# Optimization experiments

Measured on AMD Instinct MI355X. Metric: run time of the kernel, lower is better.

## Reference

```python
import jax, jax.numpy as jnp
import numpy as np

B, T, D = 2, 1024, 1024
H, DH = 16, 64          # d_head = d_model // n_heads
MAX_POS = 64


def setup_inputs() -> dict:
    key = jax.random.key(0)
    ks = jax.random.split(key, 11)
    s = 1.0 / np.sqrt(D)
    x = jax.random.normal(ks[0], (B, T, D), jnp.float32)
    Wq = jax.random.normal(ks[1], (D, D), jnp.float32) * s
    Wk = jax.random.normal(ks[2], (D, D), jnp.float32) * s
    Wv = jax.random.normal(ks[3], (D, D), jnp.float32) * s
    Wo = jax.random.normal(ks[4], (D, D), jnp.float32) * s
    bq = jnp.zeros((D,), jnp.float32)
    bk = jnp.zeros((D,), jnp.float32)
    bv = jnp.zeros((D,), jnp.float32)
    bo = jnp.zeros((D,), jnp.float32)
    pos_emb = jax.random.normal(ks[5], (H, MAX_POS, DH), jnp.float32) * 0.02
    causal_mask = jnp.triu(jnp.ones((T, T), bool), k=1)  # True = masked (j > i)
    return dict(x=x, Wq=Wq, bq=bq, Wk=Wk, bk=bk, Wv=Wv, bv=bv, Wo=Wo, bo=bo,
                pos_emb=pos_emb, causal_mask=causal_mask)


def reference(x, Wq, bq, Wk, bk, Wv, bv, Wo, bo, pos_emb, causal_mask):
    Bv, Tv, _ = x.shape
    scale = np.sqrt(DH).astype(np.float32)

    def proj(W, b):
        return (x @ W.T + b).reshape(Bv, Tv, H, DH).transpose(0, 2, 1, 3)  # (B,H,T,d)

    Q, K, V = proj(Wq, bq), proj(Wk, bk), proj(Wv, bv)

    qk = jnp.einsum('bhid,bhjd->bhij', Q, K)              # (B,H,T,T)
    gates = jax.nn.sigmoid(qk / scale)
    gates = jnp.where(causal_mask, 0.0, gates)
    cum = jnp.cumsum(gates, axis=-1)
    pos = cum[..., -1:] - cum                             # total - cumsum_left

    pos = jnp.clip(pos, 0.0, MAX_POS - 1.0)
    pos_floor = jnp.floor(pos)
    alpha = (pos - pos_floor)[..., None]                  # (B,H,T,T,1) -> broadcast
    fidx = pos_floor.astype(jnp.int32)
    cidx = jnp.clip(jnp.ceil(pos), 0, MAX_POS - 1).astype(jnp.int32)

    # q_i . PE_{i,j} via precomputed q.pos_emb table (same math, no (B,H,T,T,d) tensor)
    qpe_tab = jnp.einsum('bhid,hpd->bhip', Q, pos_emb)    # (B,H,T,MAX_POS)
    qpe_f = jnp.take_along_axis(qpe_tab, fidx, axis=-1)   # (B,H,T,T)
    qpe_c = jnp.take_along_axis(qpe_tab, cidx, axis=-1)
    q_pe = (1.0 - alpha[..., 0]) * qpe_f + alpha[..., 0] * qpe_c

    scores = (qk + q_pe) / scale
    scores = jnp.where(causal_mask, -jnp.inf, scores)
    attn = jax.nn.softmax(scores, axis=-1)

    out = jnp.einsum('bhij,bhjd->bhid', attn, V)
    out = out.transpose(0, 2, 1, 3).reshape(Bv, Tv, D)
    return out @ Wo.T + bo
```

## Files before the change

kernel.cpp:

```cpp
#include <hip/hip_runtime.h>
#include <math.h>

#define Tt 1024
#define Dd 1024
#define Hh 16
#define DHh 64
#define MAXPOS 64
#define BTt 2048

typedef short short8 __attribute__((ext_vector_type(8)));
typedef float floatx4 __attribute__((ext_vector_type(4)));

#define MFMA16 __builtin_amdgcn_mfma_f32_16x16x32_bf16

__device__ __forceinline__ unsigned short f2bf(float f) {
    unsigned u;
    __builtin_memcpy(&u, &f, 4);
    u = (u + 0x7FFFu + ((u >> 16) & 1u)) >> 16;
    return (unsigned short)u;
}
__device__ __forceinline__ float bf2fs(short s) {
    unsigned u = ((unsigned)(unsigned short)s) << 16;
    float f;
    __builtin_memcpy(&f, &u, 4);
    return f;
}
__device__ __forceinline__ float fsigm(float x) {
    return __builtin_amdgcn_rcpf(1.f + __expf(-x));
}

__global__ __launch_bounds__(256) void conv_bf16(
    const float* __restrict__ x,  const float* __restrict__ W0,
    const float* __restrict__ W1, const float* __restrict__ W2,
    const float* __restrict__ W3,
    short* __restrict__ xb, short* __restrict__ w0b, short* __restrict__ w1b,
    short* __restrict__ w2b, short* __restrict__ w3b)
{
    const float* src; short* dst; int n;
    switch (blockIdx.y) {
        case 0:  src = x;  dst = xb;  n = BTt * Dd; break;
        case 1:  src = W0; dst = w0b; n = Dd * Dd;  break;
        case 2:  src = W1; dst = w1b; n = Dd * Dd;  break;
        case 3:  src = W2; dst = w2b; n = Dd * Dd;  break;
        default: src = W3; dst = w3b; n = Dd * Dd;  break;
    }
    int idx = (blockIdx.x * 256 + threadIdx.x) * 8;
    if (idx >= n) return;
    floatx4 a0 = *(const floatx4*)&src[idx];
    floatx4 a1 = *(const floatx4*)&src[idx + 4];
    short8 s;
    for (int e = 0; e < 4; ++e) {
        s[e]     = (short)f2bf(a0[e]);
        s[e + 4] = (short)f2bf(a1[e]);
    }
    *(short8*)&dst[idx] = s;
}

#define BM 128
#define BN 128
#define BKK 64
#define LDSS 72

template <int MODE>
__device__ __forceinline__ void gemm_body(const short* __restrict__ A,
                                          const short* __restrict__ W,
                                          const float* __restrict__ bias,
                                          void* __restrict__ Cout,
                                          int N, int K)
{
    __shared__ __align__(16) short Ash[BM * LDSS];
    __shared__ __align__(16) short Bsh[BN * LDSS];
    const int t = threadIdx.x;
    const int lane = t & 63, wave = t >> 6;
    const int wm = wave >> 1, wn = wave & 1;
    const int quad = lane >> 4, l16 = lane & 15;
    const int row0 = blockIdx.x * BM, col0 = blockIdx.y * BN;

    floatx4 acc[4][4];
    for (int a = 0; a < 4; ++a)
        for (int b2 = 0; b2 < 4; ++b2)
            acc[a][b2] = (floatx4){0.f, 0.f, 0.f, 0.f};

    for (int kb = 0; kb < K; kb += BKK) {
        __syncthreads();
        for (int q2 = 0; q2 < 4; ++q2) {
            int ch = t + 256 * q2;
            int r = ch >> 3, c = ch & 7;
            *(short8*)&Ash[r * LDSS + c * 8] =
                *(const short8*)&A[(size_t)(row0 + r) * K + kb + c * 8];
            *(short8*)&Bsh[r * LDSS + c * 8] =
                *(const short8*)&W[(size_t)(col0 + r) * K + kb + c * 8];
        }
        __syncthreads();
        for (int ks = 0; ks < BKK / 32; ++ks) {
            short8 af[4], bfr[4];
            for (int tm = 0; tm < 4; ++tm)
                af[tm] = *(short8*)&Ash[(wm * 64 + tm * 16 + l16) * LDSS + ks * 32 + quad * 8];
            for (int tn = 0; tn < 4; ++tn)
                bfr[tn] = *(short8*)&Bsh[(wn * 64 + tn * 16 + l16) * LDSS + ks * 32 + quad * 8];
            for (int tm = 0; tm < 4; ++tm)
                for (int tn = 0; tn < 4; ++tn)
                    acc[tm][tn] = MFMA16(af[tm], bfr[tn], acc[tm][tn], 0, 0, 0);
        }
    }
    for (int tm = 0; tm < 4; ++tm)
        for (int tn = 0; tn < 4; ++tn) {
            int col = col0 + wn * 64 + tn * 16 + l16;
            float bv = bias[col];
            for (int r = 0; r < 4; ++r) {
                int row = row0 + wm * 64 + tm * 16 + quad * 4 + r;
                float v = acc[tm][tn][r] + bv;
                if (MODE == 0) ((float*)Cout)[(size_t)row * N + col] = v;
                else           ((short*)Cout)[(size_t)row * N + col] = (short)f2bf(v);
            }
        }
}

__global__ __launch_bounds__(256) void gemm_qkv(
    const short* __restrict__ xb,
    const short* __restrict__ Wqb, const short* __restrict__ Wkb,
    const short* __restrict__ Wvb,
    const float* __restrict__ bq, const float* __restrict__ bk,
    const float* __restrict__ bv,
    short* __restrict__ Qb, short* __restrict__ Kb, short* __restrict__ Vrow)
{
    if (blockIdx.z == 0)      gemm_body<1>(xb, Wqb, bq, Qb, Dd, Dd);
    else if (blockIdx.z == 1) gemm_body<1>(xb, Wkb, bk, Kb, Dd, Dd);
    else                      gemm_body<1>(xb, Wvb, bv, Vrow, Dd, Dd);
}

__global__ __launch_bounds__(256) void gemm_o(
    const short* __restrict__ A, const short* __restrict__ W,
    const float* __restrict__ bias, float* __restrict__ C)
{
    gemm_body<0>(A, W, bias, C, Dd, Dd);
}

__global__ __launch_bounds__(256) void vt_gates(
    const short* __restrict__ Q, const short* __restrict__ K,
    const short* __restrict__ Vrow, short* __restrict__ Vt,
    float* __restrict__ gts)
{
    __shared__ __align__(16) short Qt[32 * 72];
    __shared__ __align__(16) short KV[128 * 72];
    __shared__ float redg[32 * 4];

    const int t = threadIdx.x;

    if (blockIdx.x >= 256) {
        const int j0 = (blockIdx.x - 256) * 64, d0 = blockIdx.y * 64, b = blockIdx.z;
        short* L = KV;
        for (int s = 0; s < 2; ++s) {
            int c = t * 2 + s;
            int jr = c >> 3, c8 = c & 7;
            *(short8*)&L[jr * 72 + c8 * 8] =
                *(const short8*)&Vrow[((size_t)(b * Tt + j0 + jr)) * Dd + d0 + c8 * 8];
        }
        __syncthreads();
        for (int s = 0; s < 2; ++s) {
            int c = t * 2 + s;
            int dr = c >> 3, c8 = c & 7;
            short8 v;
            for (int e = 0; e < 8; ++e) v[e] = L[(c8 * 8 + e) * 72 + dr];
            *(short8*)&Vt[((size_t)(b * Dd + d0 + dr)) * Tt + j0 + c8 * 8] = v;
        }
        return;
    }

    const int it = blockIdx.x >> 3, jt = blockIdx.x & 7;
    const int h = blockIdx.y, b = blockIdx.z;
    const int i0 = it * 32, j0 = jt * 128;
    const int lane = t & 63, wave = t >> 6;
    const int quad = lane >> 4, l16 = lane & 15;

    float* g = &gts[(((size_t)(b * Hh + h)) * Tt + i0) * 8 + jt];
    if (j0 > i0 + 31) {
        if (t < 32) g[t * 8] = 0.f;
        return;
    }

    const float inv_scale = 0.125f;

    {
        int r = t >> 3, c = t & 7;
        *(short8*)&Qt[r * 72 + c * 8] =
            *(const short8*)&Q[((size_t)(b * Tt + i0 + r)) * Dd + h * DHh + c * 8];
    }
    for (int e = 0; e < 4; ++e) {
        int ch = t + 256 * e;
        int jr = ch >> 3, c = ch & 7;
        *(short8*)&KV[jr * 72 + c * 8] =
            *(const short8*)&K[((size_t)(b * Tt + j0 + jr)) * Dd + h * DHh + c * 8];
    }
    __syncthreads();

    int ntA = 2 * wave, ntB = ntA + 1;
    floatx4 c00 = {0,0,0,0}, c01 = {0,0,0,0}, c10 = {0,0,0,0}, c11 = {0,0,0,0};
    for (int ks = 0; ks < 2; ++ks) {
        short8 a0 = *(short8*)&Qt[(l16) * 72 + ks * 32 + quad * 8];
        short8 a1 = *(short8*)&Qt[(16 + l16) * 72 + ks * 32 + quad * 8];
        short8 b0 = *(short8*)&KV[(ntA * 16 + l16) * 72 + ks * 32 + quad * 8];
        short8 b1 = *(short8*)&KV[(ntB * 16 + l16) * 72 + ks * 32 + quad * 8];
        c00 = MFMA16(a0, b0, c00, 0, 0, 0);
        c01 = MFMA16(a0, b1, c01, 0, 0, 0);
        c10 = MFMA16(a1, b0, c10, 0, 0, 0);
        c11 = MFMA16(a1, b1, c11, 0, 0, 0);
    }
    const int jA = j0 + ntA * 16 + l16;
    const int jB = j0 + ntB * 16 + l16;
    for (int r = 0; r < 4; ++r) {
        int m0 = i0 + quad * 4 + r;
        int m1 = m0 + 16;
        float v0 = ((jA <= m0) ? fsigm(c00[r] * inv_scale) : 0.f)
                 + ((jB <= m0) ? fsigm(c01[r] * inv_scale) : 0.f);
        float v1 = ((jA <= m1) ? fsigm(c10[r] * inv_scale) : 0.f)
                 + ((jB <= m1) ? fsigm(c11[r] * inv_scale) : 0.f);
        for (int o = 1; o < 16; o <<= 1) {
            v0 += __shfl_xor(v0, o, 64);
            v1 += __shfl_xor(v1, o, 64);
        }
        if (l16 == 0) {
            redg[(quad * 4 + r) * 4 + wave]      = v0;
            redg[(16 + quad * 4 + r) * 4 + wave] = v1;
        }
    }
    __syncthreads();
    if (t < 32) {
        float s2 = redg[t * 4] + redg[t * 4 + 1] + redg[t * 4 + 2] + redg[t * 4 + 3];
        g[t * 8] = s2;
    }
}

__global__ __launch_bounds__(256) void cope_attn(
    const short* __restrict__ Q, const short* __restrict__ K,
    const short* __restrict__ Vt, const float* __restrict__ PE,
    const float* __restrict__ gts, short* __restrict__ AOb)
{
    const int h = blockIdx.y, b = blockIdx.z;
    const int t = threadIdx.x, lane = t & 63, wave = t >> 6;
    const int quad = lane >> 4, l16 = lane & 15;

    __shared__ __align__(16) short SldS[32 * 264];
    __shared__ __align__(16) short KV[128 * 72];
    __shared__ short qpeB[32 * 68];
    __shared__ float lrow[32];
    float* Sld = (float*)SldS;

    const float inv_scale = 0.125f;
    const int sr = t >> 3, ss = t & 7;

    for (int phase = 0; phase < 2; ++phase) {
        const int it = (phase == 0) ? (31 - (int)blockIdx.x) : (int)blockIdx.x;
        const int i0 = it * 32;
        const int irow = i0 + sr;

        float grow[8];
        {
            const float* gp = &gts[(((size_t)(b * Hh + h)) * Tt + i0 + sr) * 8];
            for (int k = 0; k < 8; ++k) grow[k] = gp[k];
        }
        float tot = 0.f;
        for (int k = 0; k < 8; ++k) tot += grow[k];

        short* QtS = SldS;
        {
            int r = t >> 3, c = t & 7;
            *(short8*)&QtS[r * 72 + c * 8] =
                *(const short8*)&Q[((size_t)(b * Tt + i0 + r)) * Dd + h * DHh + c * 8];
        }
        for (int e = 0; e < 16; ++e) {
            int idx = t + 256 * e;
            int p = idx >> 6, d = idx & 63;
            KV[p * 72 + d] = (short)f2bf(PE[((size_t)h * MAXPOS + p) * DHh + d]);
        }
        __syncthreads();

        short8 qa[2][2];
        for (int rb = 0; rb < 2; ++rb)
            for (int ks = 0; ks < 2; ++ks)
                qa[rb][ks] = *(short8*)&QtS[(rb * 16 + l16) * 72 + ks * 32 + quad * 8];

        {
            int mt = wave >> 1;
            int ntA = 2 * (wave & 1), ntB = ntA + 1;
            floatx4 c0f = {0, 0, 0, 0}, c1f = {0, 0, 0, 0};
            for (int ks = 0; ks < 2; ++ks) {
                short8 b0 = *(short8*)&KV[(ntA * 16 + l16) * 72 + ks * 32 + quad * 8];
                short8 b1 = *(short8*)&KV[(ntB * 16 + l16) * 72 + ks * 32 + quad * 8];
                c0f = MFMA16(qa[mt][ks], b0, c0f, 0, 0, 0);
                c1f = MFMA16(qa[mt][ks], b1, c1f, 0, 0, 0);
            }
            for (int r = 0; r < 4; ++r) {
                qpeB[(mt * 16 + quad * 4 + r) * 68 + ntA * 16 + l16] = (short)f2bf(c0f[r]);
                qpeB[(mt * 16 + quad * 4 + r) * 68 + ntB * 16 + l16] = (short)f2bf(c1f[r]);
            }
        }

        const int JT = (i0 + 159) >> 7;
        floatx4 o0 = {0, 0, 0, 0}, o1 = {0, 0, 0, 0};
        const int pv_mt = wave >> 1;
        const int pv_ntA = 2 * (wave & 1), pv_ntB = pv_ntA + 1;
        float l_acc = 0.f;
        float baseAcc = 0.f;

        short8 kreg[4];
        for (int e = 0; e < 4; ++e) {
            int ch = t + 256 * e;
            int jr = ch >> 3, c = ch & 7;
            kreg[e] = *(const short8*)&K[((size_t)(b * Tt + jr)) * Dd + h * DHh + c * 8];
        }

        for (int jt = 0; jt < JT; ++jt) {
            const int j0 = jt * 128;
            __syncthreads();
            for (int e = 0; e < 4; ++e) {
                int ch = t + 256 * e;
                int jr = ch >> 3, c = ch & 7;
                *(short8*)&KV[jr * 72 + c * 8] = kreg[e];
            }
            __syncthreads();
            {
                int ntA = 2 * wave, ntB = ntA + 1;
                floatx4 c00 = {0,0,0,0}, c01 = {0,0,0,0}, c10 = {0,0,0,0}, c11 = {0,0,0,0};
                for (int ks = 0; ks < 2; ++ks) {
                    short8 b0 = *(short8*)&KV[(ntA * 16 + l16) * 72 + ks * 32 + quad * 8];
                    short8 b1 = *(short8*)&KV[(ntB * 16 + l16) * 72 + ks * 32 + quad * 8];
                    c00 = MFMA16(qa[0][ks], b0, c00, 0, 0, 0);
                    c01 = MFMA16(qa[0][ks], b1, c01, 0, 0, 0);
                    c10 = MFMA16(qa[1][ks], b0, c10, 0, 0, 0);
                    c11 = MFMA16(qa[1][ks], b1, c11, 0, 0, 0);
                }
                for (int r = 0; r < 4; ++r) {
                    Sld[(quad * 4 + r) * 132 + ntA * 16 + l16] = c00[r];
                    Sld[(quad * 4 + r) * 132 + ntB * 16 + l16] = c01[r];
                    Sld[(16 + quad * 4 + r) * 132 + ntA * 16 + l16] = c10[r];
                    Sld[(16 + quad * 4 + r) * 132 + ntB * 16 + l16] = c11[r];
                }
            }
            __syncthreads();
            short8 vreg[4];
            for (int e = 0; e < 4; ++e) {
                int ch = t + 256 * e;
                int d = ch >> 4, c = ch & 15;
                vreg[e] = *(const short8*)&Vt[((size_t)(b * Dd + h * DHh + d)) * Tt + j0 + c * 8];
            }
            if (jt + 1 < JT) {
                for (int e = 0; e < 4; ++e) {
                    int ch = t + 256 * e;
                    int jr = ch >> 3, c = ch & 7;
                    kreg[e] = *(const short8*)&K[((size_t)(b * Tt + j0 + 128 + jr)) * Dd + h * DHh + c * 8];
                }
            }
            {
                floatx4 qv[4];
                for (int q4 = 0; q4 < 4; ++q4) {
                    short8 qraw = *(short8*)&SldS[sr * 264 + ss * 32 + q4 * 8];
                    __builtin_memcpy(&qv[q4], &qraw, 16);
                }
                float gt[16];
                float gs = 0.f;
                for (int e = 0; e < 16; ++e) {
                    int j = j0 + ss * 16 + e;
                    float qk = qv[e >> 2][e & 3];
                    float g = (j <= irow) ? fsigm(qk * inv_scale) : 0.f;
                    gt[e] = g;
                    gs += g;
                }
                float inc = gs;
                for (int d2 = 1; d2 < 8; d2 <<= 1) {
                    float n = __shfl_up(inc, d2, 64);
                    if ((lane & 7) >= d2) inc += n;
                }
                float base = baseAcc + (inc - gs);
                float run = 0.f;
                short8 p0, p1;
                for (int e = 0; e < 16; ++e) {
                    run += gt[e];
                    int j = j0 + ss * 16 + e;
                    float pos = tot - (base + run);
                    pos = fminf(fmaxf(pos, 0.f), 63.f);
                    float pf = floorf(pos);
                    float al = pos - pf;
                    int fi = (int)pf;
                    int ci = fi + 1; if (ci > 63) ci = 63;
                    float qp = (1.f - al) * bf2fs(qpeB[sr * 68 + fi]) + al * bf2fs(qpeB[sr * 68 + ci]);
                    float qk = qv[e >> 2][e & 3];
                    float p = (j <= irow) ? __expf((qk + qp) * inv_scale) : 0.f;
                    if (e < 8) p0[e] = (short)f2bf(p); else p1[e - 8] = (short)f2bf(p);
                    l_acc += p;
                }
                *(short8*)&SldS[sr * 264 + ss * 32]     = p0;
                *(short8*)&SldS[sr * 264 + ss * 32 + 8] = p1;
                baseAcc += grow[jt];
            }
            for (int e = 0; e < 4; ++e) {
                int ch = t + 256 * e;
                int d = ch >> 4, c = ch & 15;
                *(short8*)&KV[d * 136 + c * 8] = vreg[e];
            }
            __syncthreads();
            for (int ks = 0; ks < 4; ++ks) {
                short8 a  = *(short8*)&SldS[(pv_mt * 16 + l16) * 264 + ks * 64
                                            + ((quad >> 1) << 5) + ((quad & 1) << 3)];
                short8 b0 = *(short8*)&KV[(pv_ntA * 16 + l16) * 136 + ks * 32 + quad * 8];
                short8 b1 = *(short8*)&KV[(pv_ntB * 16 + l16) * 136 + ks * 32 + quad * 8];
                o0 = MFMA16(a, b0, o0, 0, 0, 0);
                o1 = MFMA16(a, b1, o1, 0, 0, 0);
            }
        }
        float lr = l_acc;
        for (int d2 = 4; d2 >= 1; d2 >>= 1) lr += __shfl_xor(lr, d2, 64);
        if (ss == 0) lrow[sr] = lr;
        __syncthreads();
        for (int r = 0; r < 4; ++r) {
            int row = pv_mt * 16 + quad * 4 + r;
            float inv = __builtin_amdgcn_rcpf(lrow[row]);
            size_t off = ((size_t)(b * Tt + i0 + row)) * Dd + h * DHh;
            AOb[off + pv_ntA * 16 + l16] = (short)f2bf(o0[r] * inv);
            AOb[off + pv_ntB * 16 + l16] = (short)f2bf(o1[r] * inv);
        }
    }
}

extern "C" void kernel_launch(void* const* d_in, const int* in_sizes, int n_in,
                              void* d_out, int out_size, void* d_ws, size_t ws_size,
                              hipStream_t stream)
{
    const float* x  = (const float*)d_in[0];
    const float* Wq = (const float*)d_in[1];
    const float* bq = (const float*)d_in[2];
    const float* Wk = (const float*)d_in[3];
    const float* bk = (const float*)d_in[4];
    const float* Wv = (const float*)d_in[5];
    const float* bv = (const float*)d_in[6];
    const float* Wo = (const float*)d_in[7];
    const float* bo = (const float*)d_in[8];
    const float* pe = (const float*)d_in[9];

    short* xb   = (short*)d_ws;
    short* Wqb  = xb   + (size_t)BTt * Dd;
    short* Wkb  = Wqb  + (size_t)Dd * Dd;
    short* Wvb  = Wkb  + (size_t)Dd * Dd;
    short* Wob  = Wvb  + (size_t)Dd * Dd;
    short* Qb   = Wob  + (size_t)Dd * Dd;
    short* Kb   = Qb   + (size_t)BTt * Dd;
    short* Vrow = Kb   + (size_t)BTt * Dd;
    short* Vtg  = Vrow + (size_t)BTt * Dd;
    short* AOb  = Vtg  + (size_t)BTt * Dd;
    float* gts  = (float*)(AOb + (size_t)BTt * Dd);

    dim3 gc(BTt * Dd / 8 / 256, 5);
    conv_bf16<<<gc, 256, 0, stream>>>(x, Wq, Wk, Wv, Wo, xb, Wqb, Wkb, Wvb, Wob);

    dim3 gq(BTt / BM, Dd / BN, 3);
    gemm_qkv<<<gq, 256, 0, stream>>>(xb, Wqb, Wkb, Wvb, bq, bk, bv, Qb, Kb, Vrow);

    dim3 gg(272, Hh, 2);
    vt_gates<<<gg, 256, 0, stream>>>(Qb, Kb, Vrow, Vtg, gts);

    dim3 ga(Tt / 32 / 2, Hh, 2);
    cope_attn<<<ga, 256, 0, stream>>>(Qb, Kb, Vtg, pe, gts, AOb);

    dim3 go(BTt / BM, Dd / BN, 1);
    gemm_o<<<go, 256, 0, stream>>>(AOb, Wob, bo, (float*)d_out);
}
```

Baseline: 200.9 us.

## Iterate key tiles right-to-left to compute suffix gate sums inline

```diff
diff --git a/kernel.cpp b/kernel.cpp
--- a/kernel.cpp
+++ b/kernel.cpp
@@ -136,105 +136,32 @@
     gemm_body<0>(A, W, bias, C, Dd, Dd);
 }
 
-__global__ __launch_bounds__(256) void vt_gates(
-    const short* __restrict__ Q, const short* __restrict__ K,
-    const short* __restrict__ Vrow, short* __restrict__ Vt,
-    float* __restrict__ gts)
-{
-    __shared__ __align__(16) short Qt[32 * 72];
-    __shared__ __align__(16) short KV[128 * 72];
-    __shared__ float redg[32 * 4];
-
+__global__ __launch_bounds__(256) void v_transpose(
+    const short* __restrict__ Vrow, short* __restrict__ Vt)
+{
+    __shared__ __align__(16) short L[64 * 72];
     const int t = threadIdx.x;
-
-    if (blockIdx.x >= 256) {
-        const int j0 = (blockIdx.x - 256) * 64, d0 = blockIdx.y * 64, b = blockIdx.z;
-        short* L = KV;
-        for (int s = 0; s < 2; ++s) {
-            int c = t * 2 + s;
-            int jr = c >> 3, c8 = c & 7;
-            *(short8*)&L[jr * 72 + c8 * 8] =
-                *(const short8*)&Vrow[((size_t)(b * Tt + j0 + jr)) * Dd + d0 + c8 * 8];
-        }
-        __syncthreads();
-        for (int s = 0; s < 2; ++s) {
-            int c = t * 2 + s;
-            int dr = c >> 3, c8 = c & 7;
-            short8 v;
-            for (int e = 0; e < 8; ++e) v[e] = L[(c8 * 8 + e) * 72 + dr];
-            *(short8*)&Vt[((size_t)(b * Dd + d0 + dr)) * Tt + j0 + c8 * 8] = v;
-        }
-        return;
-    }
-
-    const int it = blockIdx.x >> 3, jt = blockIdx.x & 7;
-    const int h = blockIdx.y, b = blockIdx.z;
-    const int i0 = it * 32, j0 = jt * 128;
-    const int lane = t & 63, wave = t >> 6;
-    const int quad = lane >> 4, l16 = lane & 15;
-
-    float* g = &gts[(((size_t)(b * Hh + h)) * Tt + i0) * 8 + jt];
-    if (j0 > i0 + 31) {
-        if (t < 32) g[t * 8] = 0.f;
-        return;
-    }
-
-    const float inv_scale = 0.125f;
-
-    {
-        int r = t >> 3, c = t & 7;
-        *(short8*)&Qt[r * 72 + c * 8] =
-            *(const short8*)&Q[((size_t)(b * Tt + i0 + r)) * Dd + h * DHh + c * 8];
-    }
-    for (int e = 0; e < 4; ++e) {
-        int ch = t + 256 * e;
-        int jr = ch >> 3, c = ch & 7;
-        *(short8*)&KV[jr * 72 + c * 8] =
-            *(const short8*)&K[((size_t)(b * Tt + j0 + jr)) * Dd + h * DHh + c * 8];
+    const int j0 = blockIdx.x * 64, d0 = blockIdx.y * 64, b = blockIdx.z;
+    for (int s = 0; s < 2; ++s) {
+        int c = t * 2 + s;
+        int jr = c >> 3, c8 = c & 7;
+        *(short8*)&L[jr * 72 + c8 * 8] =
+            *(const short8*)&Vrow[((size_t)(b * Tt + j0 + jr)) * Dd + d0 + c8 * 8];
     }
     __syncthreads();
-
-    int ntA = 2 * wave, ntB = ntA + 1;
-    floatx4 c00 = {0,0,0,0}, c01 = {0,0,0,0}, c10 = {0,0,0,0}, c11 = {0,0,0,0};
-    for (int ks = 0; ks < 2; ++ks) {
-        short8 a0 = *(short8*)&Qt[(l16) * 72 + ks * 32 + quad * 8];
-        short8 a1 = *(short8*)&Qt[(16 + l16) * 72 + ks * 32 + quad * 8];
-        short8 b0 = *(short8*)&KV[(ntA * 16 + l16) * 72 + ks * 32 + quad * 8];
-        short8 b1 = *(short8*)&KV[(ntB * 16 + l16) * 72 + ks * 32 + quad * 8];
-        c00 = MFMA16(a0, b0, c00, 0, 0, 0);
-        c01 = MFMA16(a0, b1, c01, 0, 0, 0);
-        c10 = MFMA16(a1, b0, c10, 0, 0, 0);
-        c11 = MFMA16(a1, b1, c11, 0, 0, 0);
-    }
-    const int jA = j0 + ntA * 16 + l16;
-    const int jB = j0 + ntB * 16 + l16;
-    for (int r = 0; r < 4; ++r) {
-        int m0 = i0 + quad * 4 + r;
-        int m1 = m0 + 16;
-        float v0 = ((jA <= m0) ? fsigm(c00[r] * inv_scale) : 0.f)
-                 + ((jB <= m0) ? fsigm(c01[r] * inv_scale) : 0.f);
-        float v1 = ((jA <= m1) ? fsigm(c10[r] * inv_scale) : 0.f)
-                 + ((jB <= m1) ? fsigm(c11[r] * inv_scale) : 0.f);
-        for (int o = 1; o < 16; o <<= 1) {
-            v0 += __shfl_xor(v0, o, 64);
-            v1 += __shfl_xor(v1, o, 64);
-        }
-        if (l16 == 0) {
-            redg[(quad * 4 + r) * 4 + wave]      = v0;
-            redg[(16 + quad * 4 + r) * 4 + wave] = v1;
-        }
-    }
-    __syncthreads();
-    if (t < 32) {
-        float s2 = redg[t * 4] + redg[t * 4 + 1] + redg[t * 4 + 2] + redg[t * 4 + 3];
-        g[t * 8] = s2;
+    for (int s = 0; s < 2; ++s) {
+        int c = t * 2 + s;
+        int dr = c >> 3, c8 = c & 7;
+        short8 v;
+        for (int e = 0; e < 8; ++e) v[e] = L[(c8 * 8 + e) * 72 + dr];
+        *(short8*)&Vt[((size_t)(b * Dd + d0 + dr)) * Tt + j0 + c8 * 8] = v;
     }
 }
 
 __global__ __launch_bounds__(256) void cope_attn(
     const short* __restrict__ Q, const short* __restrict__ K,
     const short* __restrict__ Vt, const float* __restrict__ PE,
-    const float* __restrict__ gts, short* __restrict__ AOb)
+    short* __restrict__ AOb)
 {
     const int h = blockIdx.y, b = blockIdx.z;
     const int t = threadIdx.x, lane = t & 63, wave = t >> 6;
@@ -253,14 +180,6 @@
         const int it = (phase == 0) ? (31 - (int)blockIdx.x) : (int)blockIdx.x;
         const int i0 = it * 32;
         const int irow = i0 + sr;
-
-        float grow[8];
-        {
-            const float* gp = &gts[(((size_t)(b * Hh + h)) * Tt + i0 + sr) * 8];
-            for (int k = 0; k < 8; ++k) grow[k] = gp[k];
-        }
-        float tot = 0.f;
-        for (int k = 0; k < 8; ++k) tot += grow[k];
 
         short* QtS = SldS;
         {
@@ -301,16 +220,16 @@
         const int pv_mt = wave >> 1;
         const int pv_ntA = 2 * (wave & 1), pv_ntB = pv_ntA + 1;
         float l_acc = 0.f;
-        float baseAcc = 0.f;
+        float rightAcc = 0.f;
 
         short8 kreg[4];
         for (int e = 0; e < 4; ++e) {
             int ch = t + 256 * e;
             int jr = ch >> 3, c = ch & 7;
-            kreg[e] = *(const short8*)&K[((size_t)(b * Tt + jr)) * Dd + h * DHh + c * 8];
-        }
-
-        for (int jt = 0; jt < JT; ++jt) {
+            kreg[e] = *(const short8*)&K[((size_t)(b * Tt + (JT - 1) * 128 + jr)) * Dd + h * DHh + c * 8];
+        }
+
+        for (int jt = JT - 1; jt >= 0; --jt) {
             const int j0 = jt * 128;
             __syncthreads();
             for (int e = 0; e < 4; ++e) {
@@ -344,11 +263,11 @@
                 int d = ch >> 4, c = ch & 15;
                 vreg[e] = *(const short8*)&Vt[((size_t)(b * Dd + h * DHh + d)) * Tt + j0 + c * 8];
             }
-            if (jt + 1 < JT) {
+            if (jt > 0) {
                 for (int e = 0; e < 4; ++e) {
                     int ch = t + 256 * e;
                     int jr = ch >> 3, c = ch & 7;
-                    kreg[e] = *(const short8*)&K[((size_t)(b * Tt + j0 + 128 + jr)) * Dd + h * DHh + c * 8];
+                    kreg[e] = *(const short8*)&K[((size_t)(b * Tt + j0 - 128 + jr)) * Dd + h * DHh + c * 8];
                 }
             }
             {
@@ -368,16 +287,17 @@
                 }
                 float inc = gs;
                 for (int d2 = 1; d2 < 8; d2 <<= 1) {
-                    float n = __shfl_up(inc, d2, 64);
-                    if ((lane & 7) >= d2) inc += n;
-                }
-                float base = baseAcc + (inc - gs);
+                    float n = __shfl_down(inc, d2, 64);
+                    if ((lane & 7) + d2 < 8) inc += n;
+                }
+                float tileTot = __shfl(inc, lane & 56, 64);
+                float base = rightAcc + (inc - gs);
                 float run = 0.f;
                 short8 p0, p1;
-                for (int e = 0; e < 16; ++e) {
+                for (int e = 15; e >= 0; --e) {
+                    int j = j0 + ss * 16 + e;
+                    float pos = base + run;
                     run += gt[e];
-                    int j = j0 + ss * 16 + e;
-                    float pos = tot - (base + run);
                     pos = fminf(fmaxf(pos, 0.f), 63.f);
                     float pf = floorf(pos);
                     float al = pos - pf;
@@ -391,7 +311,7 @@
                 }
                 *(short8*)&SldS[sr * 264 + ss * 32]     = p0;
                 *(short8*)&SldS[sr * 264 + ss * 32 + 8] = p1;
-                baseAcc += grow[jt];
+                rightAcc += tileTot;
             }
             for (int e = 0; e < 4; ++e) {
                 int ch = t + 256 * e;
@@ -447,7 +367,6 @@
     short* Vrow = Kb   + (size_t)BTt * Dd;
     short* Vtg  = Vrow + (size_t)BTt * Dd;
     short* AOb  = Vtg  + (size_t)BTt * Dd;
-    float* gts  = (float*)(AOb + (size_t)BTt * Dd);
 
     dim3 gc(BTt * Dd / 8 / 256, 5);
     conv_bf16<<<gc, 256, 0, stream>>>(x, Wq, Wk, Wv, Wo, xb, Wqb, Wkb, Wvb, Wob);
@@ -455,11 +374,11 @@
     dim3 gq(BTt / BM, Dd / BN, 3);
     gemm_qkv<<<gq, 256, 0, stream>>>(xb, Wqb, Wkb, Wvb, bq, bk, bv, Qb, Kb, Vrow);
 
-    dim3 gg(272, Hh, 2);
-    vt_gates<<<gg, 256, 0, stream>>>(Qb, Kb, Vrow, Vtg, gts);
+    dim3 gv(Tt / 64, Dd / 64, 2);
+    v_transpose<<<gv, 256, 0, stream>>>(Vrow, Vtg);
 
     dim3 ga(Tt / 32 / 2, Hh, 2);
-    cope_attn<<<ga, 256, 0, stream>>>(Qb, Kb, Vtg, pe, gts, AOb);
+    cope_attn<<<ga, 256, 0, stream>>>(Qb, Kb, Vtg, pe, AOb);
 
     dim3 go(BTt / BM, Dd / BN, 1);
     gemm_o<<<go, 256, 0, stream>>>(AOb, Wob, bo, (float*)d_out);
```

Result: faster. 182.3 us (-9.3%).
